# Kernel tuning notes

Measured on AMD Instinct MI355X. Metric: run time of the kernel, lower is better.

Reference implementation:

```python
import jax, jax.numpy as jnp
import numpy as np

K = 5
PAD = 2


def setup_inputs() -> dict:
    key = jax.random.key(0)
    k1, k2 = jax.random.split(key)
    B, C, H, W = 8, 4, 256, 256
    x = jax.random.normal(k1, (B, C, H, W), dtype=jnp.float32)
    filt = jax.random.uniform(k2, (B, C * K * K, H, W), dtype=jnp.float32)
    return {"x": x, "filt": filt}


def reference(x, filt):
    B, C, H, W = x.shape
    # identity kernel: out channel j of each group picks the j-th position of the kxk window
    eye = jnp.eye(K * K, dtype=x.dtype).reshape(K * K, 1, K, K)
    kernel = jnp.tile(eye, (C, 1, 1, 1))  # [C*K^2, 1, K, K], grouped conv = per-channel patch expand
    x_localexpand = jax.lax.conv_general_dilated(
        x, kernel,
        window_strides=(1, 1),
        padding=[(PAD, PAD), (PAD, PAD)],
        dimension_numbers=("NCHW", "OIHW", "NCHW"),
        feature_group_count=C,
    )  # [B, C*K^2, H, W]
    y = jnp.tanh(jnp.sum(x_localexpand * filt, axis=1, keepdims=True))  # [B,1,H,W]
    return y
```

## Files before the change

kernel.cpp:

```cpp
#include <hip/hip_runtime.h>
#include <math.h>

#define Hd 256
#define Wd 256
#define Cc 4
#define KK 5

typedef float v4f __attribute__((ext_vector_type(4)));

__global__ __launch_bounds__(256, 4) void dynf_kernel(const float* __restrict__ x,
                                                      const float* __restrict__ filt,
                                                      float* __restrict__ out) {
    const int bh   = blockIdx.x;
    const int b    = bh >> 8;
    const int h    = bh & 255;
    const int c    = threadIdx.x >> 6;
    const int lane = threadIdx.x & 63;
    const int w0   = lane << 2;

    const size_t HW = (size_t)Hd * Wd;
    const float* xc = x + ((size_t)b * Cc + c) * HW;
    const float* fb = filt + ((size_t)(b * (Cc * KK * KK) + c * (KK * KK))) * HW
                      + (size_t)h * Wd + w0;

    float a0 = 0.f, a1 = 0.f, a2 = 0.f, a3 = 0.f;
    const v4f vzero = {0.f, 0.f, 0.f, 0.f};

    #pragma unroll
    for (int di = 0; di < KK; ++di) {
        const int hh = h + di - 2;
        if (hh >= 0 && hh < Hd) {
            const float* xr = xc + (size_t)hh * Wd;
            v4f left  = *(const v4f*)(xr + (w0 ? (w0 - 4) : 0));
            v4f mid   = *(const v4f*)(xr + w0);
            v4f right = *(const v4f*)(xr + ((w0 + 4 < Wd) ? (w0 + 4) : 0));
            if (w0 == 0)      left  = vzero;
            if (w0 + 4 >= Wd) right = vzero;
            float xrow[8] = {left.z, left.w, mid.x, mid.y, mid.z, mid.w, right.x, right.y};

            const float* fr = fb + (size_t)(di * KK) * HW;
            #pragma unroll
            for (int dj = 0; dj < KK; ++dj) {
                v4f f = __builtin_nontemporal_load((const v4f*)(fr + (size_t)dj * HW));
                a0 = fmaf(xrow[dj + 0], f.x, a0);
                a1 = fmaf(xrow[dj + 1], f.y, a1);
                a2 = fmaf(xrow[dj + 2], f.z, a2);
                a3 = fmaf(xrow[dj + 3], f.w, a3);
            }
        }
    }

    __shared__ v4f red[Cc][64];
    v4f acc = {a0, a1, a2, a3};
    red[c][lane] = acc;
    __syncthreads();

    if (c == 0) {
        v4f s = red[0][lane] + red[1][lane] + red[2][lane] + red[3][lane];
        v4f o;
        o.x = tanhf(s.x); o.y = tanhf(s.y); o.z = tanhf(s.z); o.w = tanhf(s.w);
        __builtin_nontemporal_store(o, (v4f*)(out + (size_t)b * HW + (size_t)h * Wd + w0));
    }
}

extern "C" void kernel_launch(void* const* d_in, const int* in_sizes, int n_in,
                              void* d_out, int out_size, void* d_ws, size_t ws_size,
                              hipStream_t stream) {
    const float* x    = (const float*)d_in[0];
    const float* filt = (const float*)d_in[1];
    float* out        = (float*)d_out;

    const int grid  = 8 * 256;
    const int block = 256;
    dynf_kernel<<<grid, block, 0, stream>>>(x, filt, out);
}
```

Measured before the change: 275.9 us.

## Stage filter rows into LDS via async global_load_lds with double buffering

Filter loads now go through global_load_lds DMA into a double-buffered LDS tile, two kernel rows in flight, with manual vmcnt waits before each row is consumed. x rows are preloaded into registers first so the filter stream can be overlapped with the FMAs. The aim is better memory-level parallelism on a streaming, bandwidth-bound filter read. In exchange the kernel uses about 40KB of LDS per block, which lowers occupancy, and drops the nontemporal hint on filter loads. The hand-written waitcnt ordering is fragile.

```diff
diff --git a/kernel.cpp b/kernel.cpp
--- a/kernel.cpp
+++ b/kernel.cpp
@@ -7,6 +7,19 @@
 #define KK 5
 
 typedef float v4f __attribute__((ext_vector_type(4)));
+
+#define GLD16(gaddr, laddr)                                                          \
+    __builtin_amdgcn_global_load_lds(                                                \
+        (const __attribute__((address_space(1))) void*)(gaddr),                      \
+        (__attribute__((address_space(3))) void*)(laddr), 16, 0, 0)
+
+__device__ __forceinline__ void stage_rows(const float* __restrict__ g0, float* l0) {
+    const size_t HW = (size_t)Hd * Wd;
+#pragma unroll
+    for (int dj = 0; dj < KK; ++dj) {
+        GLD16(g0 + (size_t)dj * HW, l0 + dj * Wd);
+    }
+}
 
 __global__ __launch_bounds__(256, 4) void dynf_kernel(const float* __restrict__ x,
                                                       const float* __restrict__ filt,
@@ -19,14 +32,19 @@
     const int w0   = lane << 2;
 
     const size_t HW = (size_t)Hd * Wd;
+
+    __shared__ float lds[2][Cc][KK][Wd];
+
     const float* xc = x + ((size_t)b * Cc + c) * HW;
-    const float* fb = filt + ((size_t)(b * (Cc * KK * KK) + c * (KK * KK))) * HW
+    const float* fb = filt + ((size_t)b * (Cc * KK * KK) + (size_t)c * (KK * KK)) * HW
                       + (size_t)h * Wd + w0;
+    float* lbase = &lds[0][0][0][0];
+    float* lc0 = lbase + (size_t)c * (KK * Wd);
+    float* lc1 = lbase + (size_t)Cc * (KK * Wd) + (size_t)c * (KK * Wd);
 
-    float a0 = 0.f, a1 = 0.f, a2 = 0.f, a3 = 0.f;
+    float xrow[KK][8];
     const v4f vzero = {0.f, 0.f, 0.f, 0.f};
-
-    #pragma unroll
+#pragma unroll
     for (int di = 0; di < KK; ++di) {
         const int hh = h + di - 2;
         if (hh >= 0 && hh < Hd) {
@@ -36,27 +54,57 @@
             v4f right = *(const v4f*)(xr + ((w0 + 4 < Wd) ? (w0 + 4) : 0));
             if (w0 == 0)      left  = vzero;
             if (w0 + 4 >= Wd) right = vzero;
-            float xrow[8] = {left.z, left.w, mid.x, mid.y, mid.z, mid.w, right.x, right.y};
-
-            const float* fr = fb + (size_t)(di * KK) * HW;
-            #pragma unroll
-            for (int dj = 0; dj < KK; ++dj) {
-                v4f f = __builtin_nontemporal_load((const v4f*)(fr + (size_t)dj * HW));
-                a0 = fmaf(xrow[dj + 0], f.x, a0);
-                a1 = fmaf(xrow[dj + 1], f.y, a1);
-                a2 = fmaf(xrow[dj + 2], f.z, a2);
-                a3 = fmaf(xrow[dj + 3], f.w, a3);
-            }
+            xrow[di][0] = left.z;  xrow[di][1] = left.w;
+            xrow[di][2] = mid.x;   xrow[di][3] = mid.y;
+            xrow[di][4] = mid.z;   xrow[di][5] = mid.w;
+            xrow[di][6] = right.x; xrow[di][7] = right.y;
+        } else {
+#pragma unroll
+            for (int j = 0; j < 8; ++j) xrow[di][j] = 0.f;
         }
     }
 
-    __shared__ v4f red[Cc][64];
-    v4f acc = {a0, a1, a2, a3};
-    red[c][lane] = acc;
+    stage_rows(fb, lc0);
+    asm volatile("" ::: "memory");
+    stage_rows(fb + (size_t)KK * HW, lc1);
+    asm volatile("" ::: "memory");
+
+    float a0 = 0.f, a1 = 0.f, a2 = 0.f, a3 = 0.f;
+
+#pragma unroll
+    for (int di = 0; di < KK; ++di) {
+        if (di < KK - 1) {
+            asm volatile("s_waitcnt vmcnt(5)" ::: "memory");
+        } else {
+            asm volatile("s_waitcnt vmcnt(0)" ::: "memory");
+        }
+
+        const float* lsrc = (di & 1) ? lc1 : lc0;
+#pragma unroll
+        for (int dj = 0; dj < KK; ++dj) {
+            v4f f = *(const v4f*)(lsrc + dj * Wd + w0);
+            a0 = fmaf(xrow[di][dj + 0], f.x, a0);
+            a1 = fmaf(xrow[di][dj + 1], f.y, a1);
+            a2 = fmaf(xrow[di][dj + 2], f.z, a2);
+            a3 = fmaf(xrow[di][dj + 3], f.w, a3);
+        }
+
+        if (di + 2 < KK) {
+            asm volatile("s_waitcnt lgkmcnt(0)" ::: "memory");
+            stage_rows(fb + (size_t)(di + 2) * KK * HW, (di & 1) ? lc1 : lc0);
+            asm volatile("" ::: "memory");
+        }
+    }
+
+    __syncthreads();
+    v4f* red = (v4f*)lbase;
+    v4f acc;
+    acc.x = a0; acc.y = a1; acc.z = a2; acc.w = a3;
+    red[(size_t)c * 64 + lane] = acc;
     __syncthreads();
 
     if (c == 0) {
-        v4f s = red[0][lane] + red[1][lane] + red[2][lane] + red[3][lane];
+        v4f s = red[lane] + red[64 + lane] + red[128 + lane] + red[192 + lane];
         v4f o;
         o.x = tanhf(s.x); o.y = tanhf(s.y); o.z = tanhf(s.z); o.w = tanhf(s.w);
         __builtin_nontemporal_store(o, (v4f*)(out + (size_t)b * HW + (size_t)h * Wd + w0));
```

Measured after the change: 289.2 us. +4.8%, slower.

## Tile 8 rows per block and stream filter planes via async global-to-LDS double buffer

Applied to the files above, without the earlier changes.

Each block now handles 8 output rows, and the grid shrinks to 256 blocks with a remapped block index. The x window is loaded once into registers and reused across the 25 taps. Filter planes are streamed into a double-buffered LDS tile using global_load_lds, with manual vmcnt waits so the next plane's load overlaps the FMAs on the current one. The aim is to keep more memory requests in flight for this bandwidth-bound kernel, at the cost of only one 256-thread block per CU on a large GPU and fragile hand-written waitcnt ordering.

```diff
diff --git a/kernel.cpp b/kernel.cpp
--- a/kernel.cpp
+++ b/kernel.cpp
@@ -5,61 +5,110 @@
 #define Wd 256
 #define Cc 4
 #define KK 5
+#define HT 8
+#define XWR (HT + KK - 1)
 
 typedef float v4f __attribute__((ext_vector_type(4)));
 
-__global__ __launch_bounds__(256, 4) void dynf_kernel(const float* __restrict__ x,
+#define GLD16(gaddr, laddr)                                                          \
+    __builtin_amdgcn_global_load_lds(                                                \
+        (const __attribute__((address_space(1))) void*)(gaddr),                      \
+        (__attribute__((address_space(3))) void*)(laddr), 16, 0, 0)
+
+__global__ __launch_bounds__(256, 1) void dynf_kernel(const float* __restrict__ x,
                                                       const float* __restrict__ filt,
                                                       float* __restrict__ out) {
-    const int bh   = blockIdx.x;
-    const int b    = bh >> 8;
-    const int h    = bh & 255;
+    const int bid  = blockIdx.x;
+    const int lg   = ((bid & 7) << 5) + (bid >> 3);
+    const int b    = lg >> 5;
+    const int h0   = (lg & 31) << 3;
     const int c    = threadIdx.x >> 6;
     const int lane = threadIdx.x & 63;
     const int w0   = lane << 2;
 
     const size_t HW = (size_t)Hd * Wd;
+
+    __shared__ float lds[2][Cc][HT][Wd];
+
     const float* xc = x + ((size_t)b * Cc + c) * HW;
-    const float* fb = filt + ((size_t)(b * (Cc * KK * KK) + c * (KK * KK))) * HW
-                      + (size_t)h * Wd + w0;
+    const float* fb = filt + ((size_t)b * (Cc * KK * KK) + (size_t)c * (KK * KK)) * HW
+                      + (size_t)h0 * Wd + w0;
+    float* l0 = &lds[0][c][0][0];
+    float* l1 = &lds[1][c][0][0];
 
-    float a0 = 0.f, a1 = 0.f, a2 = 0.f, a3 = 0.f;
-    const v4f vzero = {0.f, 0.f, 0.f, 0.f};
-
-    #pragma unroll
-    for (int di = 0; di < KK; ++di) {
-        const int hh = h + di - 2;
-        if (hh >= 0 && hh < Hd) {
-            const float* xr = xc + (size_t)hh * Wd;
+    float xw[XWR][8];
+    const v4f vz = {0.f, 0.f, 0.f, 0.f};
+#pragma unroll
+    for (int ri = 0; ri < XWR; ++ri) {
+        const int g = h0 + ri - 2;
+        if (g >= 0 && g < Hd) {
+            const float* xr = xc + (size_t)g * Wd;
             v4f left  = *(const v4f*)(xr + (w0 ? (w0 - 4) : 0));
             v4f mid   = *(const v4f*)(xr + w0);
             v4f right = *(const v4f*)(xr + ((w0 + 4 < Wd) ? (w0 + 4) : 0));
-            if (w0 == 0)      left  = vzero;
-            if (w0 + 4 >= Wd) right = vzero;
-            float xrow[8] = {left.z, left.w, mid.x, mid.y, mid.z, mid.w, right.x, right.y};
-
-            const float* fr = fb + (size_t)(di * KK) * HW;
-            #pragma unroll
-            for (int dj = 0; dj < KK; ++dj) {
-                v4f f = __builtin_nontemporal_load((const v4f*)(fr + (size_t)dj * HW));
-                a0 = fmaf(xrow[dj + 0], f.x, a0);
-                a1 = fmaf(xrow[dj + 1], f.y, a1);
-                a2 = fmaf(xrow[dj + 2], f.z, a2);
-                a3 = fmaf(xrow[dj + 3], f.w, a3);
-            }
+            if (w0 == 0)      left  = vz;
+            if (w0 + 4 >= Wd) right = vz;
+            xw[ri][0] = left.z;  xw[ri][1] = left.w;
+            xw[ri][2] = mid.x;   xw[ri][3] = mid.y;
+            xw[ri][4] = mid.z;   xw[ri][5] = mid.w;
+            xw[ri][6] = right.x; xw[ri][7] = right.y;
+        } else {
+#pragma unroll
+            for (int j = 0; j < 8; ++j) xw[ri][j] = 0.f;
         }
     }
 
-    __shared__ v4f red[Cc][64];
-    v4f acc = {a0, a1, a2, a3};
-    red[c][lane] = acc;
+#pragma unroll
+    for (int r = 0; r < HT; ++r) GLD16(fb + (size_t)r * Wd, l0 + r * Wd);
+    asm volatile("" ::: "memory");
+#pragma unroll
+    for (int r = 0; r < HT; ++r) GLD16(fb + HW + (size_t)r * Wd, l1 + r * Wd);
+    asm volatile("" ::: "memory");
+
+    v4f acc[HT];
+#pragma unroll
+    for (int r = 0; r < HT; ++r) acc[r] = vz;
+
+#pragma unroll
+    for (int p = 0; p < KK * KK; ++p) {
+        if (p < KK * KK - 1) asm volatile("s_waitcnt vmcnt(8)" ::: "memory");
+        else                 asm volatile("s_waitcnt vmcnt(0)" ::: "memory");
+
+        const int di = p / KK, dj = p % KK;
+        const float* ls = (p & 1) ? l1 : l0;
+#pragma unroll
+        for (int r = 0; r < HT; ++r) {
+            v4f f = *(const v4f*)(ls + r * Wd + w0);
+            acc[r].x = fmaf(xw[r + di][0 + dj], f.x, acc[r].x);
+            acc[r].y = fmaf(xw[r + di][1 + dj], f.y, acc[r].y);
+            acc[r].z = fmaf(xw[r + di][2 + dj], f.z, acc[r].z);
+            acc[r].w = fmaf(xw[r + di][3 + dj], f.w, acc[r].w);
+        }
+
+        if (p + 2 < KK * KK) {
+            asm volatile("s_waitcnt lgkmcnt(0)" ::: "memory");
+            float* ld = (p & 1) ? l1 : l0;
+#pragma unroll
+            for (int r = 0; r < HT; ++r)
+                GLD16(fb + (size_t)(p + 2) * HW + (size_t)r * Wd, ld + r * Wd);
+            asm volatile("" ::: "memory");
+        }
+    }
+
+    __syncthreads();
+    v4f* red = (v4f*)&lds[0][0][0][0];
+#pragma unroll
+    for (int r = 0; r < HT; ++r) red[(c * HT + r) * 64 + lane] = acc[r];
     __syncthreads();
 
-    if (c == 0) {
-        v4f s = red[0][lane] + red[1][lane] + red[2][lane] + red[3][lane];
+#pragma unroll
+    for (int rr = 0; rr < 2; ++rr) {
+        const int r = c * 2 + rr;
+        v4f s = red[(0 * HT + r) * 64 + lane] + red[(1 * HT + r) * 64 + lane]
+              + red[(2 * HT + r) * 64 + lane] + red[(3 * HT + r) * 64 + lane];
         v4f o;
         o.x = tanhf(s.x); o.y = tanhf(s.y); o.z = tanhf(s.z); o.w = tanhf(s.w);
-        __builtin_nontemporal_store(o, (v4f*)(out + (size_t)b * HW + (size_t)h * Wd + w0));
+        __builtin_nontemporal_store(o, (v4f*)(out + (size_t)b * HW + (size_t)(h0 + r) * Wd + w0));
     }
 }
 
@@ -70,7 +119,7 @@
     const float* filt = (const float*)d_in[1];
     float* out        = (float*)d_out;
 
-    const int grid  = 8 * 256;
+    const int grid  = 256;
     const int block = 256;
     dynf_kernel<<<grid, block, 0, stream>>>(x, filt, out);
 }
```

After: 337.5 us. +22.3%, slower.
